# Kernel optimization log

Measured on AMD Instinct MI355X. Metric: run time of the kernel, lower is better.

## Reference

```python
import jax, jax.numpy as jnp
import numpy as np

B, W, M = 16, 32, 512
NH, HALF, K, H = 64, 32, 8, 8
LK = W // 2               # long-conv kernel size
LOUT = W - 2 * (LK - 1)   # = 2 (dilated valid conv output length)
NSP = 10                  # n_spatial (hardcoded in module)
GC1_IN = (1 + LOUT) * K   # 24


def setup_inputs() -> dict:
    key = jax.random.key(0)
    ks = jax.random.split(key, 23)
    def n(k, shp, s=0.1):
        return jax.random.normal(k, shp, jnp.float32) * s
    return dict(
        x=jax.random.normal(ks[0], (B, W, M), jnp.float32),
        adj=jax.random.uniform(ks[1], (M, M), jnp.float32) / M,  # row-normalized-ish dense adj
        Wih=n(ks[2], (NH, 1)), Whh=n(ks[3], (NH, NH)),
        bih=n(ks[4], (NH,)), bhh=n(ks[5], (NH,)),
        W1=n(ks[6], (HALF, NH)), W2=n(ks[7], (HALF, NH)), b1=n(ks[8], (HALF,)),
        V=n(ks[9], (HALF,)), bv=n(ks[10], (1,)),
        Wb=n(ks[11], (M, M)), wb=n(ks[12], (1,)),
        conv_w=n(ks[13], (K, 1, W)), conv_b=n(ks[14], (K,)),
        convl_w=n(ks[15], (K, 1, LK)), convl_b=n(ks[16], (K,)),
        gc1_w=n(ks[17], (GC1_IN, NH)), gc1_b=n(ks[18], (NH,)),
        gc2_w=n(ks[19], (NH, NSP)), gc2_b=n(ks[20], (NSP,)),
        out_w=n(ks[21], (H, NSP + NH)), out_b=n(ks[22], (H,)),
    )


def reference(x, adj, Wih, Whh, bih, bhh, W1, W2, b1, V, bv, Wb, wb,
              conv_w, conv_b, convl_w, convl_b, gc1_w, gc1_b, gc2_w, gc2_b,
              out_w, out_b):
    b = x.shape[0]
    # [b, w, m] -> per-node sequences [b*m, w]
    seq = jnp.transpose(x, (0, 2, 1)).reshape(b * M, W)

    # vanilla tanh RNN, input_size=1 (batched over all b*m series)
    inp = seq[:, :, None] * Wih[:, 0] + (bih + bhh)          # [b*m, w, nh]
    def step(h, it):
        return jnp.tanh(it + h @ Whh.T), None
    h0 = jnp.zeros((b * M, NH), x.dtype)
    last_hid, _ = jax.lax.scan(step, h0, jnp.swapaxes(inp, 0, 1))
    last_hid = last_hid.reshape(b, M, NH)                    # out_temporal

    # pairwise additive attention: a[b,i,j] = V . elu(W1 h_j + W2 h_i + b1) + bv
    e1 = last_hid @ W1.T                                     # [b, m, half] (j role)
    e2 = last_hid @ W2.T                                     # [b, m, half] (i role)
    a = jax.nn.elu(e2[:, :, None, :] + e1[:, None, :, :] + b1)  # [b,m,m,half]
    a_mx = a @ V + bv                                        # [b, m, m]
    # F.normalize(p=2, dim=1)
    norm = jnp.sqrt(jnp.sum(a_mx * a_mx, axis=1, keepdims=True))
    a_mx = a_mx / jnp.maximum(norm, 1e-12)

    # per-node short conv (kernel == window -> out len 1) as a single matmul
    r_short = seq @ conv_w[:, 0, :].T + conv_b               # [b*m, k]
    # per-node dilated long conv, batched over all b*m series
    r_long = jax.lax.conv_general_dilated(
        seq[:, None, :], convl_w, window_strides=(1,), padding='VALID',
        rhs_dilation=(2,), dimension_numbers=('NCW', 'OIW', 'NCW'))
    r_long = r_long + convl_b[None, :, None]                 # [b*m, k, LOUT]
    r = jnp.concatenate([r_short[:, :, None], r_long], axis=-1)  # [b*m, k, 1+LOUT]
    r = jax.nn.relu(r.reshape(b, M, GC1_IN))

    # gated mix of static normalized adj and learned attention adj
    c = jax.nn.sigmoid(a_mx @ Wb + wb)
    adj_mix = adj[None] * c + a_mx * (1.0 - c)               # [b, m, m]

    # two dense graph conv layers: relu(adj @ (h @ W) + b)
    h1 = jax.nn.relu(adj_mix @ (r @ gc1_w) + gc1_b)          # [b, m, nh]
    out_spatial = jax.nn.relu(adj_mix @ (h1 @ gc2_w) + gc2_b)  # [b, m, nsp]

    feat = jnp.concatenate([out_spatial, last_hid], axis=-1)  # [b, m, nsp+nh]
    out = feat @ out_w.T + out_b                              # [b, m, h]
    return jnp.transpose(out, (0, 2, 1))                      # [b, h, m]
```

## Files before the change

kernel.cpp:

```cpp
#include <hip/hip_runtime.h>


typedef __attribute__((ext_vector_type(8))) short bf16x8;
typedef __attribute__((ext_vector_type(4))) float f32x4;
#define MFMA16 __builtin_amdgcn_mfma_f32_16x16x32_bf16

__device__ __forceinline__ unsigned short f2bf(float f) {
    unsigned u = __float_as_uint(f);
    u += 0x7fff + ((u >> 16) & 1);
    return (unsigned short)(u >> 16);
}
__device__ __forceinline__ float bf2f(unsigned short h) {
    return __uint_as_float(((unsigned)h) << 16);
}
__device__ __forceinline__ float fast_tanh(float x) {
    float e = __expf(2.f * x);
    return 1.f - 2.f / (e + 1.f);
}

__global__ __launch_bounds__(256) void fused1_kernel(
    const float* __restrict__ x, const float* __restrict__ Wih,
    const float* __restrict__ Whh, const float* __restrict__ bih,
    const float* __restrict__ bhh, const float* __restrict__ W1,
    const float* __restrict__ W2, float* __restrict__ lh,
    float* __restrict__ e1, float* __restrict__ e2,
    const float* __restrict__ conv_w, const float* __restrict__ conv_b,
    const float* __restrict__ convl_w, const float* __restrict__ convl_b,
    const float* __restrict__ gc1_w, unsigned short* __restrict__ rgT,
    const float* __restrict__ Wb, unsigned short* __restrict__ WbT,
    float* __restrict__ nrmss)
{
    __shared__ __align__(16) char smem[12160];
    int blk = blockIdx.x, t = threadIdx.x;

    if (blk < 256) {
        int wid = t >> 6, lane = t & 63;
        int rowblk = blk * 32;
        int b = rowblk >> 9, mb = rowblk & 511;
        float* xs = (float*)smem;
        unsigned short* hs = (unsigned short*)(smem + 4096);
        float* rrs = (float*)(smem + 8704);

        for (int u = t; u < 1024; u += 256) {
            int tt = u >> 5, c = u & 31;
            xs[tt * 32 + c] = x[(b * 32 + tt) * 512 + mb + c];
        }
        for (int u = t; u < 2304; u += 256) hs[u] = 0;
        __syncthreads();

        if (wid < 2) {
            int l15 = lane & 15, quad = lane >> 4;
            int row0 = rowblk + wid * 16;
            unsigned short* hw0 = hs + wid * 1152;

            bf16x8 afr[4][2];
#pragma unroll
            for (int mt = 0; mt < 4; ++mt)
#pragma unroll
                for (int hf = 0; hf < 2; ++hf) {
                    const float* src = Whh + (16 * mt + l15) * 64 + 32 * hf + quad * 8;
                    union { bf16x8 v; unsigned short u[8]; } tmp;
#pragma unroll
                    for (int j = 0; j < 8; ++j) tmp.u[j] = f2bf(src[j]);
                    afr[mt][hf] = tmp.v;
                }
            bf16x8 wfr[2][2][2];
#pragma unroll
            for (int e = 0; e < 2; ++e)
#pragma unroll
                for (int nt = 0; nt < 2; ++nt)
#pragma unroll
                    for (int kf = 0; kf < 2; ++kf) {
                        const float* Wsrc = (e ? W2 : W1);
                        const float* src = Wsrc + (16 * nt + l15) * 64 + 32 * kf + quad * 8;
                        union { bf16x8 v; unsigned short u[8]; } tmp;
#pragma unroll
                        for (int j = 0; j < 8; ++j) tmp.u[j] = f2bf(src[j]);
                        wfr[e][nt][kf] = tmp.v;
                    }
            float wihv[4][4], bsv[4][4];
#pragma unroll
            for (int mt = 0; mt < 4; ++mt)
#pragma unroll
                for (int r = 0; r < 4; ++r) {
                    int n = 16 * mt + quad * 4 + r;
                    wihv[mt][r] = Wih[n];
                    bsv[mt][r]  = bih[n] + bhh[n];
                }

            float th[4][4];
            for (int tstep = 0; tstep < 32; ++tstep) {
                bf16x8 b0 = *(bf16x8*)(hw0 + l15 * 72 + quad * 8);
                bf16x8 b1 = *(bf16x8*)(hw0 + l15 * 72 + 32 + quad * 8);
                float xt = xs[tstep * 32 + wid * 16 + l15];
                f32x4 acc[4];
#pragma unroll
                for (int mt = 0; mt < 4; ++mt) {
                    f32x4 z = {0.f, 0.f, 0.f, 0.f};
                    acc[mt] = MFMA16(afr[mt][0], b0, z, 0, 0, 0);
                    acc[mt] = MFMA16(afr[mt][1], b1, acc[mt], 0, 0, 0);
                }
#pragma unroll
                for (int mt = 0; mt < 4; ++mt) {
                    ushort4 hwv;
#pragma unroll
                    for (int r = 0; r < 4; ++r)
                        th[mt][r] = fast_tanh(acc[mt][r] + xt * wihv[mt][r] + bsv[mt][r]);
                    hwv.x = f2bf(th[mt][0]); hwv.y = f2bf(th[mt][1]);
                    hwv.z = f2bf(th[mt][2]); hwv.w = f2bf(th[mt][3]);
                    *(ushort4*)(hw0 + l15 * 72 + 16 * mt + quad * 4) = hwv;
                }
            }
#pragma unroll
            for (int mt = 0; mt < 4; ++mt)
                *(float4*)(lh + (row0 + l15) * 64 + 16 * mt + quad * 4) =
                    make_float4(th[mt][0], th[mt][1], th[mt][2], th[mt][3]);

            bf16x8 a0 = *(bf16x8*)(hw0 + l15 * 72 + quad * 8);
            bf16x8 a1 = *(bf16x8*)(hw0 + l15 * 72 + 32 + quad * 8);
#pragma unroll
            for (int e = 0; e < 2; ++e) {
                float* dst = e ? e2 : e1;
#pragma unroll
                for (int nt = 0; nt < 2; ++nt) {
                    f32x4 z = {0.f, 0.f, 0.f, 0.f};
                    f32x4 ee = MFMA16(a0, wfr[e][nt][0], z, 0, 0, 0);
                    ee = MFMA16(a1, wfr[e][nt][1], ee, 0, 0, 0);
#pragma unroll
                    for (int r = 0; r < 4; ++r)
                        dst[(row0 + quad * 4 + r) * 32 + 16 * nt + l15] = ee[r];
                }
            }
        } else {
            int wid2 = wid - 2;
#pragma unroll
            for (int rep = 0; rep < 2; ++rep) {
                int task = rep * 64 + lane;
                int rl = wid2 * 16 + (task >> 3);
                int k  = task & 7;
                float s = conv_b[k];
                for (int w = 0; w < 32; ++w) s += xs[w * 32 + rl] * conv_w[k * 32 + w];
                float l0 = convl_b[k], l1 = l0;
                for (int tt = 0; tt < 16; ++tt) {
                    float wv = convl_w[k * 16 + tt];
                    l0 += xs[(2 * tt) * 32 + rl] * wv;
                    l1 += xs[(2 * tt + 1) * 32 + rl] * wv;
                }
                rrs[rl * 25 + k * 3 + 0] = fmaxf(s, 0.f);
                rrs[rl * 25 + k * 3 + 1] = fmaxf(l0, 0.f);
                rrs[rl * 25 + k * 3 + 2] = fmaxf(l1, 0.f);
            }
            __builtin_amdgcn_wave_barrier();
            int rl = wid2 * 16 + (lane & 15);
            int nb = lane >> 4;
#pragma unroll
            for (int q = 0; q < 16; ++q) {
                int n = nb * 16 + q;
                float acc = 0.f;
#pragma unroll
                for (int c = 0; c < 24; ++c) acc += rrs[rl * 25 + c] * gc1_w[c * 64 + n];
                rgT[b * 32768 + n * 512 + mb + rl] = f2bf(acc);
            }
        }
    } else if (blk < 512) {
        int bid = blk - 256;
        int nb = (bid & 15) * 32, kb = (bid >> 4) * 32;
        float* tile = (float*)smem;
        for (int u = t; u < 1024; u += 256) {
            int r = u >> 5, c = u & 31;
            tile[r * 33 + c] = Wb[(kb + r) * 512 + nb + c];
        }
        __syncthreads();
        for (int u = t; u < 1024; u += 256) {
            int r = u >> 5, c = u & 31;
            WbT[(nb + r) * 512 + kb + c] = f2bf(tile[c * 33 + r]);
        }
    } else {
        nrmss[(blk - 512) * 256 + t] = 0.f;
    }
}

__global__ __launch_bounds__(256) void amx_kernel(
    const float* __restrict__ e1, const float* __restrict__ e2,
    const float* __restrict__ b1p, const float* __restrict__ Vp,
    const float* __restrict__ bvp, unsigned short* __restrict__ amxb,
    float* __restrict__ nrmss)
{
    int bb = blockIdx.z;
    int i0 = blockIdx.y * 64, j0 = blockIdx.x * 64;
    __shared__ float e2s[64][33], e1s[64][33];
    __shared__ float Vs[32];
    __shared__ float red[16][68];
    int t = threadIdx.x;
    for (int u = t; u < 2048; u += 256) {
        int r = u >> 5, c = u & 31;
        e2s[r][c] = e2[(bb * 512 + i0 + r) * 32 + c];
        e1s[r][c] = e1[(bb * 512 + j0 + r) * 32 + c] + b1p[c];
    }
    if (t < 32) Vs[t] = Vp[t];
    __syncthreads();
    int ti = (t >> 4) * 4, tj = (t & 15) * 4;
    float acc[4][4] = {};
#pragma unroll
    for (int h = 0; h < 32; ++h) {
        float vv = Vs[h];
        float xi[4], yj[4], Exi[4], Eyj[4];
#pragma unroll
        for (int p = 0; p < 4; ++p) { xi[p] = e2s[ti + p][h]; Exi[p] = __expf(xi[p]); }
#pragma unroll
        for (int q = 0; q < 4; ++q) { yj[q] = e1s[tj + q][h]; Eyj[q] = __expf(yj[q]); }
#pragma unroll
        for (int p = 0; p < 4; ++p)
#pragma unroll
            for (int q = 0; q < 4; ++q) {
                float v = xi[p] + yj[q];
                float prod = Exi[p] * Eyj[q];
                float el = v > 0.f ? v : prod - 1.f;
                acc[p][q] += vv * el;
            }
    }
    float bv = bvp[0];
    float ss[4] = {0.f, 0.f, 0.f, 0.f};
#pragma unroll
    for (int p = 0; p < 4; ++p) {
        float v0 = acc[p][0] + bv, v1 = acc[p][1] + bv;
        float v2 = acc[p][2] + bv, v3 = acc[p][3] + bv;
        ushort4 o;
        o.x = f2bf(v0); o.y = f2bf(v1); o.z = f2bf(v2); o.w = f2bf(v3);
        *(ushort4*)(amxb + (bb * 512 + i0 + ti + p) * 512 + j0 + tj) = o;
        ss[0] += v0 * v0; ss[1] += v1 * v1; ss[2] += v2 * v2; ss[3] += v3 * v3;
    }
#pragma unroll
    for (int q = 0; q < 4; ++q) red[t >> 4][tj + q] = ss[q];
    __syncthreads();
    if (t < 64) {
        float s = 0.f;
#pragma unroll
        for (int g = 0; g < 16; ++g) s += red[g][t];
        atomicAdd(&nrmss[bb * 512 + j0 + t], s);
    }
}

__global__ __launch_bounds__(256) void gemm_adjmix_h1(
    const unsigned short* __restrict__ amxb, const unsigned short* __restrict__ WbT,
    const float* __restrict__ wbp, const float* __restrict__ adj,
    const float* __restrict__ nrmss, unsigned short* __restrict__ adjmixb,
    const unsigned short* __restrict__ rgT, const float* __restrict__ gc1_b,
    const float* __restrict__ gc2_w, float* __restrict__ h1g)
{
    const int bb = blockIdx.y;
    const int i0 = blockIdx.x * 32;
    __shared__ __align__(16) char smem[25088];
    float* rn = (float*)smem;
    short* As = (short*)(smem + 2048);
    short* Bs = (short*)(smem + 6656);
    float (*h1s)[72] = (float (*)[72])(smem + 15872);

    const int t = threadIdx.x, w = t >> 6, lane = t & 63;
    const int l15 = lane & 15, quad = lane >> 4;

    for (int u = t; u < 512; u += 256)
        rn[u] = 1.f / fmaxf(sqrtf(nrmss[bb * 512 + u]), 1e-12f);
    __syncthreads();

    const unsigned short* Ag = amxb + bb * 262144;
    const float wb = wbp[0];
    const int rowb = i0 + 16 * (w & 1);
    const int colb = 256 * (w >> 1);

    f32x4 acc[4][4] = {};
    const unsigned short* Arow = Ag + (rowb + l15) * 512;
    for (int k0 = 0; k0 < 512; k0 += 64) {
        bf16x8 a0, a1;
        {
            union { int4 v; unsigned short us[8]; } r0, r1;
            r0.v = *(const int4*)(Arow + k0 + quad * 8);
            r1.v = *(const int4*)(Arow + k0 + 32 + quad * 8);
            union { bf16x8 v; unsigned short us[8]; } o0, o1;
            const float* rn0 = rn + k0 + quad * 8;
#pragma unroll
            for (int c = 0; c < 8; ++c) {
                o0.us[c] = f2bf(bf2f(r0.us[c]) * rn0[c]);
                o1.us[c] = f2bf(bf2f(r1.us[c]) * rn0[32 + c]);
            }
            a0 = o0.v; a1 = o1.v;
        }
#pragma unroll
        for (int j64 = 0; j64 < 4; ++j64)
#pragma unroll
        for (int nt = 0; nt < 4; ++nt) {
            const unsigned short* Brow =
                WbT + (colb + j64 * 64 + nt * 16 + l15) * 512 + k0;
            bf16x8 b0 = *(const bf16x8*)(Brow + quad * 8);
            bf16x8 b1 = *(const bf16x8*)(Brow + 32 + quad * 8);
            acc[j64][nt] = MFMA16(a0, b0, acc[j64][nt], 0, 0, 0);
            acc[j64][nt] = MFMA16(a1, b1, acc[j64][nt], 0, 0, 0);
        }
    }
#pragma unroll
    for (int j64 = 0; j64 < 4; ++j64)
#pragma unroll
    for (int nt = 0; nt < 4; ++nt)
#pragma unroll
    for (int r = 0; r < 4; ++r) {
        int i = rowb + quad * 4 + r;
        int j = colb + j64 * 64 + nt * 16 + l15;
        float s  = acc[j64][nt][r] + wb;
        float cv = 1.f / (1.f + __expf(-s));
        float am = bf2f(f2bf(bf2f(Ag[i * 512 + j]) * rn[j]));
        float ad = adj[i * 512 + j];
        adjmixb[(bb * 512 + i) * 512 + j] = f2bf(ad * cv + am * (1.f - cv));
    }
    __syncthreads();

    const unsigned short* Ag2 = adjmixb + bb * 262144;
    const unsigned short* Bg2 = rgT + bb * 32768;
    const int rt = w & 1, ntb = (w >> 1) * 2;
    const int si = t >> 3, so = t & 7;
    f32x4 acc2[2] = {};
    int4 qa, qb0, qb1;
    {
        qa  = *(const int4*)(Ag2 + (i0 + si) * 512 + so * 8);
        qb0 = *(const int4*)(Bg2 + si * 512 + so * 8);
        qb1 = *(const int4*)(Bg2 + (32 + si) * 512 + so * 8);
    }
    for (int kt = 0; kt < 8; ++kt) {
        __syncthreads();
        *(int4*)(As + si * 72 + so * 8) = qa;
        *(int4*)(Bs + si * 72 + so * 8) = qb0;
        *(int4*)(Bs + (32 + si) * 72 + so * 8) = qb1;
        if (kt < 7) {
            const int k0n = (kt + 1) * 64;
            qa  = *(const int4*)(Ag2 + (i0 + si) * 512 + k0n + so * 8);
            qb0 = *(const int4*)(Bg2 + si * 512 + k0n + so * 8);
            qb1 = *(const int4*)(Bg2 + (32 + si) * 512 + k0n + so * 8);
        }
        __syncthreads();
        bf16x8 a0 = *(bf16x8*)(As + (16 * rt + l15) * 72 + quad * 8);
        bf16x8 a1 = *(bf16x8*)(As + (16 * rt + l15) * 72 + 32 + quad * 8);
#pragma unroll
        for (int q = 0; q < 2; ++q) {
            int nt = ntb + q;
            bf16x8 b0 = *(bf16x8*)(Bs + (16 * nt + l15) * 72 + quad * 8);
            bf16x8 b1 = *(bf16x8*)(Bs + (16 * nt + l15) * 72 + 32 + quad * 8);
            acc2[q] = MFMA16(a0, b0, acc2[q], 0, 0, 0);
            acc2[q] = MFMA16(a1, b1, acc2[q], 0, 0, 0);
        }
    }
#pragma unroll
    for (int q = 0; q < 2; ++q)
#pragma unroll
    for (int r = 0; r < 4; ++r) {
        int il = 16 * rt + quad * 4 + r;
        int j = 16 * (ntb + q) + l15;
        h1s[il][j] = fmaxf(acc2[q][r] + gc1_b[j], 0.f);
    }
    __syncthreads();
    for (int u = t; u < 320; u += 256) {
        int row = u / 10, ns = u - row * 10;
        float a2 = 0.f;
#pragma unroll
        for (int j = 0; j < 64; ++j) a2 += h1s[row][j] * gc2_w[j * 10 + ns];
        h1g[(bb * 512 + i0 + row) * 10 + ns] = a2;
    }
}

__global__ __launch_bounds__(256) void ospout_kernel(
    const unsigned short* __restrict__ adjmix, const float* __restrict__ h1g,
    const float* __restrict__ gc2_b, const float* __restrict__ lh,
    const float* __restrict__ out_w, const float* __restrict__ out_b,
    float* __restrict__ out)
{
    int r0 = blockIdx.x * 16;
    int bb = r0 >> 9;
    int wid = threadIdx.x >> 6, lane = threadIdx.x & 63;
    __shared__ float Bsm[10][512];
    __shared__ float ow[8][80];
    __shared__ float ob[8], g2b[10];
    for (int u = threadIdx.x; u < 5120; u += 256) {
        int k = u / 10, ns = u - k * 10;
        Bsm[ns][k] = h1g[bb * 5120 + u];
    }
    if (threadIdx.x < 8)  ob[threadIdx.x]  = out_b[threadIdx.x];
    if (threadIdx.x < 10) g2b[threadIdx.x] = gc2_b[threadIdx.x];
    for (int u = threadIdx.x; u < 592; u += 256) {
        int hh = u / 74, c = u - hh * 74;
        ow[hh][c] = out_w[u];
    }
    __syncthreads();
#pragma unroll
    for (int half = 0; half < 4; ++half) {
        int row = r0 + half * 4 + wid, m = row & 511;
        const unsigned short* Ar = adjmix + row * 512;
        float a[8];
#pragma unroll
        for (int q = 0; q < 8; ++q) a[q] = bf2f(Ar[lane + 64 * q]);
        float os[10];
#pragma unroll
        for (int ns = 0; ns < 10; ++ns) {
            float s = 0.f;
#pragma unroll
            for (int q = 0; q < 8; ++q) s += a[q] * Bsm[ns][lane + 64 * q];
#pragma unroll
            for (int off = 32; off; off >>= 1) s += __shfl_xor(s, off);
            os[ns] = fmaxf(s + g2b[ns], 0.f);
        }
        float lv = lh[row * 64 + lane];
#pragma unroll
        for (int hh = 0; hh < 8; ++hh) {
            float t1 = lv * ow[hh][10 + lane];
#pragma unroll
            for (int off = 32; off; off >>= 1) t1 += __shfl_xor(t1, off);
            if (lane == hh) {
                float acc = ob[hh] + t1;
#pragma unroll
                for (int ns = 0; ns < 10; ++ns) acc += os[ns] * ow[hh][ns];
                out[bb * 4096 + hh * 512 + m] = acc;
            }
        }
    }
}

extern "C" void kernel_launch(void* const* d_in, const int* in_sizes, int n_in,
                              void* d_out, int out_size, void* d_ws, size_t ws_size,
                              hipStream_t stream)
{
    const float* x       = (const float*)d_in[0];
    const float* adj     = (const float*)d_in[1];
    const float* Wih     = (const float*)d_in[2];
    const float* Whh     = (const float*)d_in[3];
    const float* bih     = (const float*)d_in[4];
    const float* bhh     = (const float*)d_in[5];
    const float* W1      = (const float*)d_in[6];
    const float* W2      = (const float*)d_in[7];
    const float* b1      = (const float*)d_in[8];
    const float* V       = (const float*)d_in[9];
    const float* bv      = (const float*)d_in[10];
    const float* Wb      = (const float*)d_in[11];
    const float* wb      = (const float*)d_in[12];
    const float* conv_w  = (const float*)d_in[13];
    const float* conv_b  = (const float*)d_in[14];
    const float* convl_w = (const float*)d_in[15];
    const float* convl_b = (const float*)d_in[16];
    const float* gc1_w   = (const float*)d_in[17];
    const float* gc1_b   = (const float*)d_in[18];
    const float* gc2_w   = (const float*)d_in[19];
    const float* gc2_b   = (const float*)d_in[20];
    const float* out_w   = (const float*)d_in[21];
    const float* out_b   = (const float*)d_in[22];

    float* ws    = (float*)d_ws;
    float* lh    = ws;
    float* e1    = lh + 524288;
    float* e2    = e1 + 262144;
    float* nrmss = e2 + 262144;
    float* h1g   = nrmss + 8192;
    unsigned short* amxb    = (unsigned short*)(h1g + 81920);
    unsigned short* adjmixb = amxb + 4194304;
    unsigned short* WbT     = adjmixb + 4194304;
    unsigned short* rgT     = WbT + 262144;

    fused1_kernel<<<544, 256, 0, stream>>>(
        x, Wih, Whh, bih, bhh, W1, W2, lh, e1, e2,
        conv_w, conv_b, convl_w, convl_b, gc1_w, rgT, Wb, WbT, nrmss);
    amx_kernel<<<dim3(8, 8, 16), 256, 0, stream>>>(e1, e2, b1, V, bv,
                                                   amxb, nrmss);
    gemm_adjmix_h1<<<dim3(16, 16), 256, 0, stream>>>(
        amxb, WbT, wb, adj, nrmss, adjmixb, rgT, gc1_b, gc2_w, h1g);
    ospout_kernel<<<512, 256, 0, stream>>>(adjmixb, h1g, gc2_b, lh,
                                           out_w, out_b, (float*)d_out);
}
```

Baseline: 245.0 us.

## Pre-swizzle Wb into MFMA fragment layout and halve gemm row tile

The Wb transpose now writes bf16 data in a fragment-major layout, so each lane loads its MFMA B operand as one contiguous 16-byte chunk rather than through strided row reads. The adjmix/h1 GEMM kernel now covers 16 rows per block instead of 32, which doubles the grid to 512 blocks, and each wave handles 128 columns. Launch bounds request 2 blocks per SM and shared memory shrinks. This aims to improve load coalescing and occupancy, at the cost of reading Wb twice as often across blocks and leaving half the threads idle when staging A.

```diff
diff --git a/kernel.cpp b/kernel.cpp
--- a/kernel.cpp
+++ b/kernel.cpp
@@ -27,7 +27,7 @@
     const float* __restrict__ conv_w, const float* __restrict__ conv_b,
     const float* __restrict__ convl_w, const float* __restrict__ convl_b,
     const float* __restrict__ gc1_w, unsigned short* __restrict__ rgT,
-    const float* __restrict__ Wb, unsigned short* __restrict__ WbT,
+    const float* __restrict__ Wb, unsigned short* __restrict__ WbTf,
     float* __restrict__ nrmss)
 {
     __shared__ __align__(16) char smem[12160];
@@ -173,7 +173,11 @@
         __syncthreads();
         for (int u = t; u < 1024; u += 256) {
             int r = u >> 5, c = u & 31;
-            WbT[(nb + r) * 512 + kb + c] = f2bf(tile[c * 33 + r]);
+            int j = nb + r, k = kb + c;
+            int frag = ((j >> 6) * 8 + (k >> 6)) * 8 + ((j >> 4) & 3) * 2
+                     + ((k >> 5) & 1);
+            int ln = ((k >> 3) & 3) * 16 + (j & 15);
+            WbTf[frag * 512 + ln * 8 + (k & 7)] = f2bf(tile[c * 33 + r]);
         }
     } else {
         nrmss[(blk - 512) * 256 + t] = 0.f;
@@ -241,20 +245,20 @@
     }
 }
 
-__global__ __launch_bounds__(256) void gemm_adjmix_h1(
-    const unsigned short* __restrict__ amxb, const unsigned short* __restrict__ WbT,
+__global__ __launch_bounds__(256, 2) void gemm_adjmix_h1(
+    const unsigned short* __restrict__ amxb, const unsigned short* __restrict__ WbTf,
     const float* __restrict__ wbp, const float* __restrict__ adj,
     const float* __restrict__ nrmss, unsigned short* __restrict__ adjmixb,
     const unsigned short* __restrict__ rgT, const float* __restrict__ gc1_b,
     const float* __restrict__ gc2_w, float* __restrict__ h1g)
 {
     const int bb = blockIdx.y;
-    const int i0 = blockIdx.x * 32;
-    __shared__ __align__(16) char smem[25088];
+    const int i0 = blockIdx.x * 16;
+    __shared__ __align__(16) char smem[18176];
     float* rn = (float*)smem;
     short* As = (short*)(smem + 2048);
-    short* Bs = (short*)(smem + 6656);
-    float (*h1s)[72] = (float (*)[72])(smem + 15872);
+    short* Bs = (short*)(smem + 4352);
+    float (*h1s)[72] = (float (*)[72])(smem + 13568);
 
     const int t = threadIdx.x, w = t >> 6, lane = t & 63;
     const int l15 = lane & 15, quad = lane >> 4;
@@ -265,12 +269,12 @@
 
     const unsigned short* Ag = amxb + bb * 262144;
     const float wb = wbp[0];
-    const int rowb = i0 + 16 * (w & 1);
-    const int colb = 256 * (w >> 1);
-
-    f32x4 acc[4][4] = {};
-    const unsigned short* Arow = Ag + (rowb + l15) * 512;
-    for (int k0 = 0; k0 < 512; k0 += 64) {
+    const int colb = 128 * w;
+
+    f32x4 acc[2][4] = {};
+    const unsigned short* Arow = Ag + (i0 + l15) * 512;
+    for (int k0c = 0; k0c < 8; ++k0c) {
+        const int k0 = k0c * 64;
         bf16x8 a0, a1;
         {
             union { int4 v; unsigned short us[8]; } r0, r1;
@@ -286,24 +290,26 @@
             a0 = o0.v; a1 = o1.v;
         }
 #pragma unroll
-        for (int j64 = 0; j64 < 4; ++j64)
-#pragma unroll
-        for (int nt = 0; nt < 4; ++nt) {
-            const unsigned short* Brow =
-                WbT + (colb + j64 * 64 + nt * 16 + l15) * 512 + k0;
-            bf16x8 b0 = *(const bf16x8*)(Brow + quad * 8);
-            bf16x8 b1 = *(const bf16x8*)(Brow + 32 + quad * 8);
-            acc[j64][nt] = MFMA16(a0, b0, acc[j64][nt], 0, 0, 0);
-            acc[j64][nt] = MFMA16(a1, b1, acc[j64][nt], 0, 0, 0);
-        }
-    }
-#pragma unroll
-    for (int j64 = 0; j64 < 4; ++j64)
+        for (int j64 = 0; j64 < 2; ++j64) {
+            const int jt = 2 * w + j64;
+#pragma unroll
+            for (int nt = 0; nt < 4; ++nt) {
+                const unsigned short* fr =
+                    WbTf + (((jt * 8 + k0c) * 4 + nt) * 2) * 512 + lane * 8;
+                bf16x8 b0 = *(const bf16x8*)(fr);
+                bf16x8 b1 = *(const bf16x8*)(fr + 512);
+                acc[j64][nt] = MFMA16(a0, b0, acc[j64][nt], 0, 0, 0);
+                acc[j64][nt] = MFMA16(a1, b1, acc[j64][nt], 0, 0, 0);
+            }
+        }
+    }
+#pragma unroll
+    for (int j64 = 0; j64 < 2; ++j64)
 #pragma unroll
     for (int nt = 0; nt < 4; ++nt)
 #pragma unroll
     for (int r = 0; r < 4; ++r) {
-        int i = rowb + quad * 4 + r;
+        int i = i0 + quad * 4 + r;
         int j = colb + j64 * 64 + nt * 16 + l15;
         float s  = acc[j64][nt][r] + wb;
         float cv = 1.f / (1.f + __expf(-s));
@@ -315,49 +321,40 @@
 
     const unsigned short* Ag2 = adjmixb + bb * 262144;
     const unsigned short* Bg2 = rgT + bb * 32768;
-    const int rt = w & 1, ntb = (w >> 1) * 2;
     const int si = t >> 3, so = t & 7;
-    f32x4 acc2[2] = {};
+    f32x4 acc2 = {0.f, 0.f, 0.f, 0.f};
     int4 qa, qb0, qb1;
-    {
-        qa  = *(const int4*)(Ag2 + (i0 + si) * 512 + so * 8);
-        qb0 = *(const int4*)(Bg2 + si * 512 + so * 8);
-        qb1 = *(const int4*)(Bg2 + (32 + si) * 512 + so * 8);
-    }
+    if (t < 128) qa = *(const int4*)(Ag2 + (i0 + si) * 512 + so * 8);
+    qb0 = *(const int4*)(Bg2 + si * 512 + so * 8);
+    qb1 = *(const int4*)(Bg2 + (32 + si) * 512 + so * 8);
     for (int kt = 0; kt < 8; ++kt) {
         __syncthreads();
-        *(int4*)(As + si * 72 + so * 8) = qa;
+        if (t < 128) *(int4*)(As + si * 72 + so * 8) = qa;
         *(int4*)(Bs + si * 72 + so * 8) = qb0;
         *(int4*)(Bs + (32 + si) * 72 + so * 8) = qb1;
         if (kt < 7) {
             const int k0n = (kt + 1) * 64;
-            qa  = *(const int4*)(Ag2 + (i0 + si) * 512 + k0n + so * 8);
+            if (t < 128) qa = *(const int4*)(Ag2 + (i0 + si) * 512 + k0n + so * 8);
             qb0 = *(const int4*)(Bg2 + si * 512 + k0n + so * 8);
             qb1 = *(const int4*)(Bg2 + (32 + si) * 512 + k0n + so * 8);
         }
         __syncthreads();
-        bf16x8 a0 = *(bf16x8*)(As + (16 * rt + l15) * 72 + quad * 8);
-        bf16x8 a1 = *(bf16x8*)(As + (16 * rt + l15) * 72 + 32 + quad * 8);
-#pragma unroll
-        for (int q = 0; q < 2; ++q) {
-            int nt = ntb + q;
-            bf16x8 b0 = *(bf16x8*)(Bs + (16 * nt + l15) * 72 + quad * 8);
-            bf16x8 b1 = *(bf16x8*)(Bs + (16 * nt + l15) * 72 + 32 + quad * 8);
-            acc2[q] = MFMA16(a0, b0, acc2[q], 0, 0, 0);
-            acc2[q] = MFMA16(a1, b1, acc2[q], 0, 0, 0);
-        }
-    }
-#pragma unroll
-    for (int q = 0; q < 2; ++q)
+        bf16x8 a0 = *(bf16x8*)(As + l15 * 72 + quad * 8);
+        bf16x8 a1 = *(bf16x8*)(As + l15 * 72 + 32 + quad * 8);
+        bf16x8 b0 = *(bf16x8*)(Bs + (16 * w + l15) * 72 + quad * 8);
+        bf16x8 b1 = *(bf16x8*)(Bs + (16 * w + l15) * 72 + 32 + quad * 8);
+        acc2 = MFMA16(a0, b0, acc2, 0, 0, 0);
+        acc2 = MFMA16(a1, b1, acc2, 0, 0, 0);
+    }
 #pragma unroll
     for (int r = 0; r < 4; ++r) {
-        int il = 16 * rt + quad * 4 + r;
-        int j = 16 * (ntb + q) + l15;
-        h1s[il][j] = fmaxf(acc2[q][r] + gc1_b[j], 0.f);
-    }
-    __syncthreads();
-    for (int u = t; u < 320; u += 256) {
-        int row = u / 10, ns = u - row * 10;
+        int il = quad * 4 + r;
+        int j = 16 * w + l15;
+        h1s[il][j] = fmaxf(acc2[r] + gc1_b[j], 0.f);
+    }
+    __syncthreads();
+    if (t < 160) {
+        int row = t / 10, ns = t - row * 10;
         float a2 = 0.f;
 #pragma unroll
         for (int j = 0; j < 64; ++j) a2 += h1s[row][j] * gc2_w[j * 10 + ns];
@@ -457,16 +454,16 @@
     float* h1g   = nrmss + 8192;
     unsigned short* amxb    = (unsigned short*)(h1g + 81920);
     unsigned short* adjmixb = amxb + 4194304;
-    unsigned short* WbT     = adjmixb + 4194304;
-    unsigned short* rgT     = WbT + 262144;
+    unsigned short* WbTf    = adjmixb + 4194304;
+    unsigned short* rgT     = WbTf + 262144;
 
     fused1_kernel<<<544, 256, 0, stream>>>(
         x, Wih, Whh, bih, bhh, W1, W2, lh, e1, e2,
-        conv_w, conv_b, convl_w, convl_b, gc1_w, rgT, Wb, WbT, nrmss);
+        conv_w, conv_b, convl_w, convl_b, gc1_w, rgT, Wb, WbTf, nrmss);
     amx_kernel<<<dim3(8, 8, 16), 256, 0, stream>>>(e1, e2, b1, V, bv,
                                                    amxb, nrmss);
-    gemm_adjmix_h1<<<dim3(16, 16), 256, 0, stream>>>(
-        amxb, WbT, wb, adj, nrmss, adjmixb, rgT, gc1_b, gc2_w, h1g);
+    gemm_adjmix_h1<<<dim3(32, 16), 256, 0, stream>>>(
+        amxb, WbTf, wb, adj, nrmss, adjmixb, rgT, gc1_b, gc2_w, h1g);
     ospout_kernel<<<512, 256, 0, stream>>>(adjmixb, h1g, gc2_b, lh,
                                            out_w, out_b, (float*)d_out);
 }
```

New measurement: 214.4 us. 1.14x faster.
